# Optimization experiments

Measured on AMD Instinct MI355X. Metric: run time of the kernel, lower is better.

Reference implementation:

```python
import jax, jax.numpy as jnp
import numpy as np
import math

N_LEVELS = 8
PLANE_RES = 512
FEAT_DIM = 16
N_VERT = 10
N_SAMPLES = 262144
LEVEL_OFFSET = 0.0


def _projection_matrices():
    # planotic_solid vertices for n_vertices == 10 (half-dodecahedron)
    phi = (1.0 + math.sqrt(5.0)) / 2.0
    verts = np.array([
        [1.0, 1.0, 1.0], [1.0, 1.0, -1.0], [1.0, -1.0, 1.0], [1.0, -1.0, -1.0],
        [0.0, phi, 1.0 / phi], [0.0, phi, -1.0 / phi],
        [1.0 / phi, 0.0, phi], [1.0 / phi, 0.0, -phi],
        [phi, 1.0 / phi, 0.0], [phi, -1.0 / phi, 0.0]], dtype=np.float64)
    verts /= np.linalg.norm(verts, axis=-1, keepdims=True)
    Ps = []
    for a in verts:
        if a[0] != 0 or a[1] != 0:
            p0 = np.array([-a[1], a[0], 0.0])
        else:
            p0 = np.array([0.0, -a[2], a[1]])
        p1 = np.cross(a, p0)
        p0 /= np.linalg.norm(p0)
        p1 /= np.linalg.norm(p1)
        Ps.append(np.stack([p0, p1], axis=0))
    return np.stack(Ps, axis=0).astype(np.float32)  # (V, 2, 3)

P_MATS = _projection_matrices()

# static ripmap geometry: plane (l1, l2) has shape (H = res>>l2, W = res>>l1)
_W = np.array([PLANE_RES >> l for l in range(N_LEVELS)], dtype=np.int32)
_H = _W.copy()
_SIZES = np.array([int(_H[l2]) * int(_W[l1])
                   for l1 in range(N_LEVELS) for l2 in range(N_LEVELS)], dtype=np.int64)
_OFFS = np.concatenate([[0], np.cumsum(_SIZES)[:-1]]).astype(np.int32)


def build_ripmaps_flat(fm):
    """Build the 8x8 anisotropic mip pyramid and pack all planes into one flat buffer.
    fm: (V, H, W, F). Returns (V, total_pixels, F)."""
    flats = []
    base = fm
    for l1 in range(N_LEVELS):
        if l1 > 0:
            base = 0.5 * (base[:, :, 0::2] + base[:, :, 1::2])  # AvgPool (1,2): pool width
        cur = base
        for l2 in range(N_LEVELS):
            if l2 > 0:
                cur = 0.5 * (cur[:, 0::2] + cur[:, 1::2])        # AvgPool (2,1): pool height
            flats.append(cur.reshape(N_VERT, -1, FEAT_DIM))
    return jnp.concatenate(flats, axis=1)


def multi_anisomip_interp(flat, coords, level):
    """flat: (V, T, F) packed ripmaps; coords: (N, V, 2) in [-1, 1];
    level: (N, V, 2) fractional levels in [0, L-1].
    Quadrilinear: bilinear in space x bilinear across the (l1, l2) level grid."""
    W_arr = jnp.asarray(_W)
    H_arr = jnp.asarray(_H)
    off_arr = jnp.asarray(_OFFS)
    vidx = jnp.arange(N_VERT)[None, :]
    lx, ly = level[..., 0], level[..., 1]
    l1f_f = jnp.clip(jnp.floor(lx), 0.0, N_LEVELS - 1)
    l2f_f = jnp.clip(jnp.floor(ly), 0.0, N_LEVELS - 1)
    wx = jnp.clip(lx - l1f_f, 0.0, 1.0)
    wy = jnp.clip(ly - l2f_f, 0.0, 1.0)
    l1f = l1f_f.astype(jnp.int32)
    l2f = l2f_f.astype(jnp.int32)
    l1c = jnp.minimum(l1f + 1, N_LEVELS - 1)
    l2c = jnp.minimum(l2f + 1, N_LEVELS - 1)
    enc = jnp.zeros(coords.shape[:-1] + (FEAT_DIM,), dtype=flat.dtype)
    for l1, wl1 in ((l1f, 1.0 - wx), (l1c, wx)):
        Wl = W_arr[l1]  # (N, V)
        for l2, wl2 in ((l2f, 1.0 - wy), (l2c, wy)):
            Hl = H_arr[l2]
            off = off_arr[l1 * N_LEVELS + l2]
            u = (coords[..., 0] * 0.5 + 0.5) * Wl - 0.5
            v = (coords[..., 1] * 0.5 + 0.5) * Hl - 0.5
            uf = jnp.floor(u)
            vf = jnp.floor(v)
            fu = u - uf
            fv = v - vf
            ix0 = jnp.clip(uf.astype(jnp.int32), 0, Wl - 1)
            ix1 = jnp.clip(uf.astype(jnp.int32) + 1, 0, Wl - 1)
            iy0 = jnp.clip(vf.astype(jnp.int32), 0, Hl - 1)
            iy1 = jnp.clip(vf.astype(jnp.int32) + 1, 0, Hl - 1)
            wl = wl1 * wl2
            for ix, iy, wc in ((ix0, iy0, (1 - fu) * (1 - fv)),
                               (ix1, iy0, fu * (1 - fv)),
                               (ix0, iy1, (1 - fu) * fv),
                               (ix1, iy1, fu * fv)):
                idx = off + iy * Wl + ix  # (N, V) flat pixel index
                enc = enc + (wl * wc)[..., None] * flat[vidx, idx]
    return enc  # (N, V, F)


def setup_inputs() -> dict:
    key = jax.random.key(0)
    k1, k2, k3 = jax.random.split(key, 3)
    means = jax.random.uniform(k1, (N_SAMPLES, 3), minval=-1.0, maxval=1.0, dtype=jnp.float32)
    A = jax.random.normal(k2, (N_SAMPLES, 3, 3), dtype=jnp.float32) * 0.02
    covs = jnp.einsum('nij,nkj->nik', A, A) + 1e-10 * jnp.eye(3, dtype=jnp.float32)
    fm = jax.random.uniform(k3, (N_VERT, PLANE_RES, PLANE_RES, FEAT_DIM),
                            minval=-0.01, maxval=0.01, dtype=jnp.float32)
    return {"means": means, "covs": covs, "fm": fm}


def reference(means, covs, fm):
    P = jnp.asarray(P_MATS)                                   # (V, 2, 3)
    means_proj = jnp.einsum('nd,vcd->nvc', means, P)          # (N, V, 2)
    sig2 = jnp.einsum('vad,nde,vae->nva', P, covs, P)         # diag of P C P^T, (N, V, 2)
    sigmas = jnp.sqrt(jnp.maximum(sig2, 1e-20))
    level = jnp.log2(sigmas) + LEVEL_OFFSET + math.log2(PLANE_RES)
    level = jnp.clip(level, 0.0, N_LEVELS - 1)
    flat = build_ripmaps_flat(fm)
    enc = multi_anisomip_interp(flat, means_proj, level)      # (N, V, F)
    return enc.reshape(means.shape[0], N_VERT * FEAT_DIM)
```

## Files before the change

kernel.cpp:

```cpp
#include <hip/hip_runtime.h>
#include <hip/hip_fp16.h>


#define NV 10
#define FD 16
#define NS 262144
#define HALF_NS 131072
#define PYR_PX 1040400L
#define PYR_BYTES 332928000L
#define DUP0_PX 10404000
#define DUP_VPX 57600
#define OFF_PL 351360000L

__constant__ float c_P[NV][2][3] = {
  {{-0.7071067811865476f, 0.7071067811865476f, 0.0f},
   {-0.4082482904638631f,-0.4082482904638631f, 0.8164965809277261f}},
  {{-0.7071067811865476f, 0.7071067811865476f, 0.0f},
   { 0.4082482904638631f, 0.4082482904638631f, 0.8164965809277261f}},
  {{ 0.7071067811865476f, 0.7071067811865476f, 0.0f},
   {-0.4082482904638631f, 0.4082482904638631f, 0.8164965809277261f}},
  {{ 0.7071067811865476f, 0.7071067811865476f, 0.0f},
   { 0.4082482904638631f,-0.4082482904638631f, 0.8164965809277261f}},
  {{-1.0f, 0.0f, 0.0f},
   { 0.0f,-0.3568220897730899f, 0.9341723589627157f}},
  {{-1.0f, 0.0f, 0.0f},
   { 0.0f, 0.3568220897730899f, 0.9341723589627157f}},
  {{ 0.0f, 1.0f, 0.0f},
   {-0.9341723589627157f, 0.0f, 0.3568220897730899f}},
  {{ 0.0f, 1.0f, 0.0f},
   { 0.9341723589627157f, 0.0f, 0.3568220897730899f}},
  {{-0.3568220897730899f, 0.9341723589627157f, 0.0f},
   { 0.0f, 0.0f, 1.0f}},
  {{ 0.3568220897730899f, 0.9341723589627157f, 0.0f},
   { 0.0f, 0.0f, 1.0f}},
};

__constant__ int c_CW[8] = {0, 512, 768, 896, 960, 992, 1008, 1016};

__device__ __forceinline__ int offp_a(int l1, int l2) {
  return 1044480 - (1020 << (10 - l1)) + ((1024 - (1024 >> l2)) << (9 - l1));
}

__device__ __forceinline__ uint4 havg(uint4 a, uint4 c, __half2 hhalf) {
  uint4 res;
  __half2* rr = (__half2*)&res;
  const __half2* ha = (const __half2*)&a;
  const __half2* hc = (const __half2*)&c;
  #pragma unroll
  for (int j = 0; j < 4; ++j) rr[j] = __hmul2(__hadd2(ha[j], hc[j]), hhalf);
  return res;
}

__global__ __launch_bounds__(256) void build_all(const float* __restrict__ fm,
                                                 __half* __restrict__ pyr)
{
  __shared__ uint4 ldsA[2048];
  __shared__ uint4 ldsB[1024];
  int bid = blockIdx.x;
  int v = bid >> 8;
  int rem = bid & 255;
  int b = rem >> 2;
  int s = rem & 3;
  int t = threadIdx.x;

  __half* bv = pyr + (long)v * PYR_PX * FD;
  uint4* bv4 = (uint4*)bv;
  const __half2 hhalf = __floats2half2_rn(0.5f, 0.5f);

  {
    const float4* src = (const float4*)(fm +
        (((long)v * 512 + b * 8) * 512 + s * 128) * FD);
    uint2* ldsu2 = (uint2*)ldsA;
    #pragma unroll
    for (int i = 0; i < 16; ++i) {
      int u = t + 256 * i;
      int r = u >> 9;
      int f4 = u & 511;
      int px = f4 >> 2, qq = f4 & 3;
      float4 d = src[(long)r * 2048 + f4];
      __half2 h0 = __floats2half2_rn(d.x, d.y);
      __half2 h1 = __floats2half2_rn(d.z, d.w);
      uint2 val;
      val.x = *(unsigned*)&h0; val.y = *(unsigned*)&h1;
      ldsu2[(r * 128 + px) * 4 + qq] = val;
    }
  }
  __syncthreads();

  #pragma unroll
  for (int l1 = 0; l1 < 8; ++l1) {
    uint4* cur = (l1 & 1) ? ldsB : ldsA;
    const int Wc = 128 >> l1;

    if (l1 < 7) {
      uint4* nxt = (l1 & 1) ? ldsA : ldsB;
      const int Wn = Wc >> 1;
      const int units = 8 * Wn * 2;
      const int Wgn = 512 >> (l1 + 1);
      const int colbase = offp_a(l1 + 1, 0) + s * Wn;
      for (int u = t; u < units; u += 256) {
        int k = u & 1;
        int xr = u >> 1;
        int x = xr & (Wn - 1);
        int r = xr >> (6 - l1);
        uint4 a = cur[(r * Wc + 2 * x) * 2 + k];
        uint4 c = cur[(r * Wc + 2 * x + 1) * 2 + k];
        uint4 res = havg(a, c, hhalf);
        nxt[(r * Wn + x) * 2 + k] = res;
        bv4[(long)(colbase + (b * 8 + r) * Wgn + x) * 2 + k] = res;
      }
    }

    {
      const int slots = Wc * 2;
      if (t < slots) {
        int k = t & 1, x = t >> 1;
        const int Wg = 512 >> l1;
        uint4 r0 = cur[(0 * Wc + x) * 2 + k];
        uint4 r1 = cur[(1 * Wc + x) * 2 + k];
        uint4 r2 = cur[(2 * Wc + x) * 2 + k];
        uint4 r3 = cur[(3 * Wc + x) * 2 + k];
        uint4 r4 = cur[(4 * Wc + x) * 2 + k];
        uint4 r5 = cur[(5 * Wc + x) * 2 + k];
        uint4 r6 = cur[(6 * Wc + x) * 2 + k];
        uint4 r7 = cur[(7 * Wc + x) * 2 + k];
        uint4 a0 = havg(r0, r1, hhalf), a1 = havg(r2, r3, hhalf);
        uint4 a2 = havg(r4, r5, hhalf), a3 = havg(r6, r7, hhalf);
        uint4 b0 = havg(a0, a1, hhalf), b1 = havg(a2, a3, hhalf);
        uint4 c0 = havg(b0, b1, hhalf);
        int gx = s * Wc + x;
        long p1 = (long)offp_a(l1, 1) + (long)(b * 4) * Wg + gx;
        bv4[p1 * 2 + k] = a0;
        bv4[(p1 + Wg) * 2 + k] = a1;
        bv4[(p1 + 2 * Wg) * 2 + k] = a2;
        bv4[(p1 + 3 * Wg) * 2 + k] = a3;
        long p2 = (long)offp_a(l1, 2) + (long)(b * 2) * Wg + gx;
        bv4[p2 * 2 + k] = b0;
        bv4[(p2 + Wg) * 2 + k] = b1;
        long p3 = (long)offp_a(l1, 3) + (long)b * Wg + gx;
        bv4[p3 * 2 + k] = c0;
      }
    }
    __syncthreads();
  }
}

template<int L2SRC, int NLEV>
__global__ __launch_bounds__(256) void pool_hN(__half* __restrict__ pyr)
{
  constexpr int R = 1 << NLEV;
  constexpr int HL = 512 >> (L2SRC + NLEV);
  int total = NV * HL * 2040;
  int t = blockIdx.x * 256 + threadIdx.x;
  if (t >= total) return;
  int u = t % 2040;
  int r2 = t / 2040;
  int c = u >> 1, k = u & 1;
  int y = r2 % HL;
  int v = r2 / HL;
  int l1 = 0;
  #pragma unroll
  for (int i = 1; i < 8; ++i) l1 += (c >= c_CW[i]) ? 1 : 0;
  int x = c - c_CW[l1];
  int W = 512 >> l1;
  __half* bv = pyr + (long)v * PYR_PX * FD;
  const __half* src = bv + (long)offp_a(l1, L2SRC) * FD;

  uint4 d[R];
  long base = ((long)(y * R) * W + x) * FD + k * 8;
  #pragma unroll
  for (int r = 0; r < R; ++r)
    d[r] = *(const uint4*)(src + base + (long)r * W * FD);

  const __half2 hhalf = __floats2half2_rn(0.5f, 0.5f);
  #pragma unroll
  for (int lev = 1; lev <= NLEV; ++lev) {
    int cnt = R >> lev;
    __half* dst = bv + (long)offp_a(l1, L2SRC + lev) * FD;
    #pragma unroll
    for (int r = 0; r < cnt; ++r) {
      d[r] = havg(d[2 * r], d[2 * r + 1], hhalf);
      *(uint4*)(dst + (((long)(y * cnt + r)) * W + x) * FD + k * 8) = d[r];
    }
  }
}

__global__ __launch_bounds__(256) void build_dup(__half* __restrict__ pyr)
{
  int cb = blockIdx.y;
  int l1 = 2 + (cb >> 2), l2 = 2 + (cb & 3);
  int W = 512 >> l1, H = 512 >> l2;
  int units = NV * W * H * 2;
  int gx = blockIdx.x * 256 + threadIdx.x;
  if (gx >= units) return;
  int k = gx & 1;
  int p = gx >> 1;
  int x = p & (W - 1);
  int r = p >> (9 - l1);
  int y = r & (H - 1);
  int v = r >> (9 - l2);
  long srcPx = (long)v * PYR_PX + offp_a(l1, l2) + y * W + min(x + 1, W - 1);
  int Ad = 61440 - (245760 >> l1);
  int Bd = 256 - (1024 >> l2);
  long dstPx = (long)DUP0_PX + (long)v * DUP_VPX + Ad + ((Bd + y) << (9 - l1)) + x;
  const uint4* src = (const uint4*)(pyr + srcPx * FD);
  uint4* dst = (uint4*)(pyr + dstPx * FD);
  dst[k] = src[k];
}

__global__ __launch_bounds__(256) void proj_kernel(const float* __restrict__ means,
                                                   const float* __restrict__ covs,
                                                   float4* __restrict__ pl)
{
  int n = blockIdx.x * 256 + threadIdx.x;
  if (n >= NS) return;
  float m0 = means[3 * n], m1 = means[3 * n + 1], m2 = means[3 * n + 2];
  const float* C = covs + 9L * n;
  float c0 = C[0], c1 = C[1], c2 = C[2];
  float c3 = C[3], c4 = C[4], c5 = C[5];
  float c6 = C[6], c7 = C[7], c8 = C[8];
  #pragma unroll
  for (int v = 0; v < NV; ++v) {
    float p00 = c_P[v][0][0], p01 = c_P[v][0][1], p02 = c_P[v][0][2];
    float p10 = c_P[v][1][0], p11 = c_P[v][1][1], p12 = c_P[v][1][2];
    float cx = m0 * p00 + m1 * p01 + m2 * p02;
    float cy = m0 * p10 + m1 * p11 + m2 * p12;
    float t0 = c0 * p00 + c1 * p01 + c2 * p02;
    float t1 = c3 * p00 + c4 * p01 + c5 * p02;
    float t2 = c6 * p00 + c7 * p01 + c8 * p02;
    float s2x = p00 * t0 + p01 * t1 + p02 * t2;
    t0 = c0 * p10 + c1 * p11 + c2 * p12;
    t1 = c3 * p10 + c4 * p11 + c5 * p12;
    t2 = c6 * p10 + c7 * p11 + c8 * p12;
    float s2y = p10 * t0 + p11 * t1 + p12 * t2;
    float lx = 0.5f * log2f(fmaxf(s2x, 1e-20f)) + 9.0f;
    float ly = 0.5f * log2f(fmaxf(s2y, 1e-20f)) + 9.0f;
    lx = fminf(fmaxf(lx, 0.0f), 7.0f);
    ly = fminf(fmaxf(ly, 0.0f), 7.0f);
    pl[(long)v * NS + n] = make_float4(cx, cy, lx, ly);
  }
}

struct Ctx {
  int oA, oB, oC, oD, oE, oF, oG, oH;
  __half2 wA, wB, wC, wD, wE, wF, wG, wH;
  int z00;
  float fwA, fwB;
  int ix0, iy0, dy0;
};

__device__ __forceinline__ Ctx mk_ctx(const float4 p, const bool qodd,
                                      const int dupRel)
{
  Ctx c;
  float cx = p.x, cy = p.y, lx = p.z, ly = p.w;
  int l1f = (int)lx, l2f = (int)ly;
  float wx = lx - (float)l1f, wy = ly - (float)l2f;
  int l1c = min(l1f + 1, 7);
  int l2c = min(l2f + 1, 7);

  int sh_0 = 9 - l1f;
  int Ar_0 = 1044480 - (1020 << (10 - l1f));
  float u0 = (cx * 0.5f + 0.5f) * (float)(1 << sh_0) - 0.5f;
  float uf0 = floorf(u0);
  float fu0 = u0 - uf0;
  int iu0 = (int)uf0;
  bool e0 = (iu0 < 0) || (iu0 >= (1 << sh_0) - 1);
  int ix_0 = min(max(iu0, 0), (1 << sh_0) - 1);
  float wxl_0 = qodd ? (e0 ? 0.0f : fu0) : (e0 ? 1.0f : 1.0f - fu0);
  int pOdd_0 = ix_0 & 1;
  int Ad_0 = 61440 - (245760 >> l1f);
  int inR1_0 = ((unsigned)(l1f - 2) <= 3u) ? 1 : 0;

  int sh_1 = 9 - l1c;
  int Ar_1 = 1044480 - (1020 << (10 - l1c));
  float u1 = (cx * 0.5f + 0.5f) * (float)(1 << sh_1) - 0.5f;
  float uf1 = floorf(u1);
  float fu1 = u1 - uf1;
  int iu1 = (int)uf1;
  bool e1 = (iu1 < 0) || (iu1 >= (1 << sh_1) - 1);
  int ix_1 = min(max(iu1, 0), (1 << sh_1) - 1);
  float wxl_1 = qodd ? (e1 ? 0.0f : fu1) : (e1 ? 1.0f : 1.0f - fu1);
  int pOdd_1 = ix_1 & 1;
  int Ad_1 = 61440 - (245760 >> l1c);
  int inR1_1 = ((unsigned)(l1c - 2) <= 3u) ? 1 : 0;

  float wl1_0 = 1.0f - wx, wl1_1 = wx;

  int H0 = 512 >> l2f;
  float vv0 = (cy * 0.5f + 0.5f) * (float)H0 - 0.5f;
  float vf0 = floorf(vv0);
  float fv_0 = vv0 - vf0;
  int iv0 = (int)vf0;
  int iy_0 = min(max(iv0, 0), H0 - 1);
  int dy_0 = min(max(iv0 + 1, 0), H0 - 1) - iy_0;
  int Bv_0 = 1024 - (1024 >> l2f);
  int Bd_0 = 256 - (1024 >> l2f);
  int inR2_0 = ((unsigned)(l2f - 2) <= 3u) ? 1 : 0;

  int H1 = 512 >> l2c;
  float vv1 = (cy * 0.5f + 0.5f) * (float)H1 - 0.5f;
  float vf1 = floorf(vv1);
  float fv_1 = vv1 - vf1;
  int iv1 = (int)vf1;
  int iy_1 = min(max(iv1, 0), H1 - 1);
  int dy_1 = min(max(iv1 + 1, 0), H1 - 1) - iy_1;
  int Bv_1 = 1024 - (1024 >> l2c);
  int Bd_1 = 256 - (1024 >> l2c);
  int inR2_1 = ((unsigned)(l2c - 2) <= 3u) ? 1 : 0;

  float wl2_0 = 1.0f - wy, wl2_1 = wy;

  bool s00 = pOdd_0 && inR1_0 && inR2_0;
  c.oA = s00 ? (dupRel + Ad_0 + ((Bd_0 + iy_0) << sh_0) + ix_0 - 1)
             : (Ar_0 + ((Bv_0 + iy_0) << sh_0) + ix_0);
  c.oB = c.oA + (dy_0 << sh_0);
  bool s01 = pOdd_0 && inR1_0 && inR2_1;
  c.oC = s01 ? (dupRel + Ad_0 + ((Bd_1 + iy_1) << sh_0) + ix_0 - 1)
             : (Ar_0 + ((Bv_1 + iy_1) << sh_0) + ix_0);
  c.oD = c.oC + (dy_1 << sh_0);
  bool s10 = pOdd_1 && inR1_1 && inR2_0;
  c.oE = s10 ? (dupRel + Ad_1 + ((Bd_0 + iy_0) << sh_1) + ix_1 - 1)
             : (Ar_1 + ((Bv_0 + iy_0) << sh_1) + ix_1);
  c.oF = c.oE + (dy_0 << sh_1);
  bool s11 = pOdd_1 && inR1_1 && inR2_1;
  c.oG = s11 ? (dupRel + Ad_1 + ((Bd_1 + iy_1) << sh_1) + ix_1 - 1)
             : (Ar_1 + ((Bv_1 + iy_1) << sh_1) + ix_1);
  c.oH = c.oG + (dy_1 << sh_1);

  float wb00 = wl1_0 * wl2_0 * wxl_0;
  float wb01 = wl1_0 * wl2_1 * wxl_0;
  float wb10 = wl1_1 * wl2_0 * wxl_1;
  float wb11 = wl1_1 * wl2_1 * wxl_1;
  c.wA = __float2half2_rn(wb00 * (1.0f - fv_0));
  c.wB = __float2half2_rn(wb00 * fv_0);
  c.wC = __float2half2_rn(wb01 * (1.0f - fv_1));
  c.wD = __float2half2_rn(wb01 * fv_1);
  c.wE = __float2half2_rn(wb10 * (1.0f - fv_0));
  c.wF = __float2half2_rn(wb10 * fv_0);
  c.wG = __float2half2_rn(wb11 * (1.0f - fv_1));
  c.wH = __float2half2_rn(wb11 * fv_1);

  c.z00 = ((l1f | l2f) == 0) ? 1 : 0;
  c.fwA = wb00 * (1.0f - fv_0);
  c.fwB = wb00 * fv_0;
  c.ix0 = ix_0; c.iy0 = iy_0; c.dy0 = dy_0;
  if (c.z00) {
    __half2 z = __float2half2_rn(0.0f);
    c.wA = z; c.wB = z;
  }
  return c;
}

__global__ __launch_bounds__(256) void interp8(const float4* __restrict__ pl,
                                               const __half* __restrict__ pyr,
                                               const float* __restrict__ fm,
                                               float* __restrict__ out)
{
  int bid = blockIdx.x;
  int swz = (bid & 7) * 2560 + (bid >> 3);
  int t = swz * 256 + threadIdx.x;
  int q = t & 3;
  bool qodd = (q & 1);
  int vlow = (t >> 2) & 1;
  int n = (t >> 3) & (HALF_NS - 1);
  int v2 = t >> 20;
  int v = v2 * 2 + vlow;
  int nA = n, nB = n + HALF_NS;
  int dupRel = DUP0_PX + v * DUP_VPX - v * 1040400;

  float4 pA = pl[(long)v * NS + nA];
  float4 pB = pl[(long)v * NS + nB];

  const __half* bvq = pyr + (long)v * PYR_PX * FD + ((q & 1) * 16 + (q >> 1) * 8);

  Ctx cA = mk_ctx(pA, qodd, dupRel);
  uint4 dAA = *(const uint4*)(bvq + (long)cA.oA * FD);
  uint4 dAB = *(const uint4*)(bvq + (long)cA.oB * FD);
  uint4 dAC = *(const uint4*)(bvq + (long)cA.oC * FD);
  uint4 dAD = *(const uint4*)(bvq + (long)cA.oD * FD);
  uint4 dAE = *(const uint4*)(bvq + (long)cA.oE * FD);
  uint4 dAF = *(const uint4*)(bvq + (long)cA.oF * FD);
  uint4 dAG = *(const uint4*)(bvq + (long)cA.oG * FD);
  uint4 dAH = *(const uint4*)(bvq + (long)cA.oH * FD);

  Ctx cB = mk_ctx(pB, qodd, dupRel);
  uint4 dBA = *(const uint4*)(bvq + (long)cB.oA * FD);
  uint4 dBB = *(const uint4*)(bvq + (long)cB.oB * FD);
  uint4 dBC = *(const uint4*)(bvq + (long)cB.oC * FD);
  uint4 dBD = *(const uint4*)(bvq + (long)cB.oD * FD);
  uint4 dBE = *(const uint4*)(bvq + (long)cB.oE * FD);
  uint4 dBF = *(const uint4*)(bvq + (long)cB.oF * FD);
  uint4 dBG = *(const uint4*)(bvq + (long)cB.oG * FD);
  uint4 dBH = *(const uint4*)(bvq + (long)cB.oH * FD);
  __builtin_amdgcn_sched_barrier(0);

  __half2 z = __float2half2_rn(0.0f);
  __half2 aA0 = z, aA1 = z, aA2 = z, aA3 = z;
  __half2 aB0 = z, aB1 = z, aB2 = z, aB3 = z;
  #define ACC8(A0, A1, A2, A3, D, W) { const __half2* hh = (const __half2*)&(D); \
    A0 = __hfma2(hh[0], (W), A0); A1 = __hfma2(hh[1], (W), A1);                   \
    A2 = __hfma2(hh[2], (W), A2); A3 = __hfma2(hh[3], (W), A3); }
  ACC8(aA0,aA1,aA2,aA3, dAA, cA.wA) ACC8(aA0,aA1,aA2,aA3, dAB, cA.wB)
  ACC8(aA0,aA1,aA2,aA3, dAC, cA.wC) ACC8(aA0,aA1,aA2,aA3, dAD, cA.wD)
  ACC8(aA0,aA1,aA2,aA3, dAE, cA.wE) ACC8(aA0,aA1,aA2,aA3, dAF, cA.wF)
  ACC8(aA0,aA1,aA2,aA3, dAG, cA.wG) ACC8(aA0,aA1,aA2,aA3, dAH, cA.wH)
  ACC8(aB0,aB1,aB2,aB3, dBA, cB.wA) ACC8(aB0,aB1,aB2,aB3, dBB, cB.wB)
  ACC8(aB0,aB1,aB2,aB3, dBC, cB.wC) ACC8(aB0,aB1,aB2,aB3, dBD, cB.wD)
  ACC8(aB0,aB1,aB2,aB3, dBE, cB.wE) ACC8(aB0,aB1,aB2,aB3, dBF, cB.wF)
  ACC8(aB0,aB1,aB2,aB3, dBG, cB.wG) ACC8(aB0,aB1,aB2,aB3, dBH, cB.wH)
  #undef ACC8

  const float* fmv = fm + (long)v * (262144L * FD) + (q >> 1) * 8;
  if (cA.z00) {
    int px = min(cA.ix0 + (qodd ? 1 : 0), 511);
    long o0 = ((long)cA.iy0 * 512 + px) * FD;
    long o1 = o0 + (long)cA.dy0 * 512 * FD;
    float4 ga = *(const float4*)(fmv + o0);
    float4 gb = *(const float4*)(fmv + o0 + 4);
    float4 ha = *(const float4*)(fmv + o1);
    float4 hb = *(const float4*)(fmv + o1 + 4);
    __half2 hw0 = __float2half2_rn(cA.fwA);
    __half2 hw1 = __float2half2_rn(cA.fwB);
    aA0 = __hfma2(__floats2half2_rn(ga.x, ga.y), hw0, aA0);
    aA1 = __hfma2(__floats2half2_rn(ga.z, ga.w), hw0, aA1);
    aA2 = __hfma2(__floats2half2_rn(gb.x, gb.y), hw0, aA2);
    aA3 = __hfma2(__floats2half2_rn(gb.z, gb.w), hw0, aA3);
    aA0 = __hfma2(__floats2half2_rn(ha.x, ha.y), hw1, aA0);
    aA1 = __hfma2(__floats2half2_rn(ha.z, ha.w), hw1, aA1);
    aA2 = __hfma2(__floats2half2_rn(hb.x, hb.y), hw1, aA2);
    aA3 = __hfma2(__floats2half2_rn(hb.z, hb.w), hw1, aA3);
  }
  if (cB.z00) {
    int px = min(cB.ix0 + (qodd ? 1 : 0), 511);
    long o0 = ((long)cB.iy0 * 512 + px) * FD;
    long o1 = o0 + (long)cB.dy0 * 512 * FD;
    float4 ga = *(const float4*)(fmv + o0);
    float4 gb = *(const float4*)(fmv + o0 + 4);
    float4 ha = *(const float4*)(fmv + o1);
    float4 hb = *(const float4*)(fmv + o1 + 4);
    __half2 hw0 = __float2half2_rn(cB.fwA);
    __half2 hw1 = __float2half2_rn(cB.fwB);
    aB0 = __hfma2(__floats2half2_rn(ga.x, ga.y), hw0, aB0);
    aB1 = __hfma2(__floats2half2_rn(ga.z, ga.w), hw0, aB1);
    aB2 = __hfma2(__floats2half2_rn(gb.x, gb.y), hw0, aB2);
    aB3 = __hfma2(__floats2half2_rn(gb.z, gb.w), hw0, aB3);
    aB0 = __hfma2(__floats2half2_rn(ha.x, ha.y), hw1, aB0);
    aB1 = __hfma2(__floats2half2_rn(ha.z, ha.w), hw1, aB1);
    aB2 = __hfma2(__floats2half2_rn(hb.x, hb.y), hw1, aB2);
    aB3 = __hfma2(__floats2half2_rn(hb.z, hb.w), hw1, aB3);
  }

  #define XC(A0, A1, A2, A3) {                                   \
    int x0 = *(int*)&A0, x1 = *(int*)&A1;                        \
    int x2 = *(int*)&A2, x3 = *(int*)&A3;                        \
    int y0 = __shfl_xor(x0, 1), y1 = __shfl_xor(x1, 1);          \
    int y2 = __shfl_xor(x2, 1), y3 = __shfl_xor(x3, 1);          \
    A0 = __hadd2(A0, *(__half2*)&y0); A1 = __hadd2(A1, *(__half2*)&y1); \
    A2 = __hadd2(A2, *(__half2*)&y2); A3 = __hadd2(A3, *(__half2*)&y3); }
  XC(aA0, aA1, aA2, aA3)
  XC(aB0, aB1, aB2, aB3)
  #undef XC

  __half2 sA0 = qodd ? aA2 : aA0;
  __half2 sA1 = qodd ? aA3 : aA1;
  float2 fA0 = __half22float2(sA0);
  float2 fA1 = __half22float2(sA1);
  *(float4*)(out + ((long)nA * NV + v) * FD + q * 4) =
      make_float4(fA0.x, fA0.y, fA1.x, fA1.y);

  __half2 sB0 = qodd ? aB2 : aB0;
  __half2 sB1 = qodd ? aB3 : aB1;
  float2 fB0 = __half22float2(sB0);
  float2 fB1 = __half22float2(sB1);
  *(float4*)(out + ((long)nB * NV + v) * FD + q * 4) =
      make_float4(fB0.x, fB0.y, fB1.x, fB1.y);
}

extern "C" void kernel_launch(void* const* d_in, const int* in_sizes, int n_in,
                              void* d_out, int out_size, void* d_ws, size_t ws_size,
                              hipStream_t stream)
{
  const float* means = (const float*)d_in[0];
  const float* covs  = (const float*)d_in[1];
  const float* fm    = (const float*)d_in[2];
  float* out = (float*)d_out;
  __half* pyr = (__half*)d_ws;
  float4* pl  = (float4*)((char*)d_ws + OFF_PL);

  build_all<<<NV * 256, 256, 0, stream>>>(fm, pyr);
  {
    int tB = NV * 8 * 2040;
    pool_hN<3, 3><<<(tB + 255) / 256, 256, 0, stream>>>(pyr);
    int tC = NV * 4 * 2040;
    pool_hN<6, 1><<<(tC + 255) / 256, 256, 0, stream>>>(pyr);
  }
  {
    dim3 g(1280, 16, 1);
    build_dup<<<g, 256, 0, stream>>>(pyr);
  }
  proj_kernel<<<(NS + 255) / 256, 256, 0, stream>>>(means, covs, pl);

  interp8<<<20480, 256, 0, stream>>>(pl, pyr, fm, out);
}
```

Baseline: 251.2 us.

## Skip building level-0 ripmap rows; handle low-level samples in a fixup pass

Stops writing the l1=0 and l2=0 pyramid planes (full-resolution column and row mips), which cuts pyramid construction traffic. Samples whose level is below 1 on either axis are collected into a list with a global atomic in the projection kernel. A new fixup kernel then recomputes those samples by averaging directly from the fp32 feature map, and the main interpolation kernel zeroes the weights that would have read the missing planes. The cost is atomic contention, an extra kernel, and per-sample strided gathers that loop over up to 128 source texels for coarse levels.

```diff
diff --git a/kernel.cpp b/kernel.cpp
--- a/kernel.cpp
+++ b/kernel.cpp
@@ -7,10 +7,11 @@
 #define NS 262144
 #define HALF_NS 131072
 #define PYR_PX 1040400L
-#define PYR_BYTES 332928000L
 #define DUP0_PX 10404000
 #define DUP_VPX 57600
-#define OFF_PL 351360000L
+#define OFF_PL   351360000L
+#define OFF_CNT  393303040L
+#define OFF_LIST 393303104L
 
 __constant__ float c_P[NV][2][3] = {
   {{-0.7071067811865476f, 0.7071067811865476f, 0.0f},
@@ -96,8 +97,6 @@
       uint4* nxt = (l1 & 1) ? ldsA : ldsB;
       const int Wn = Wc >> 1;
       const int units = 8 * Wn * 2;
-      const int Wgn = 512 >> (l1 + 1);
-      const int colbase = offp_a(l1 + 1, 0) + s * Wn;
       for (int u = t; u < units; u += 256) {
         int k = u & 1;
         int xr = u >> 1;
@@ -105,13 +104,11 @@
         int r = xr >> (6 - l1);
         uint4 a = cur[(r * Wc + 2 * x) * 2 + k];
         uint4 c = cur[(r * Wc + 2 * x + 1) * 2 + k];
-        uint4 res = havg(a, c, hhalf);
-        nxt[(r * Wn + x) * 2 + k] = res;
-        bv4[(long)(colbase + (b * 8 + r) * Wgn + x) * 2 + k] = res;
+        nxt[(r * Wn + x) * 2 + k] = havg(a, c, hhalf);
       }
     }
 
-    {
+    if (l1 >= 1) {
       const int slots = Wc * 2;
       if (t < slots) {
         int k = t & 1, x = t >> 1;
@@ -150,12 +147,12 @@
 {
   constexpr int R = 1 << NLEV;
   constexpr int HL = 512 >> (L2SRC + NLEV);
-  int total = NV * HL * 2040;
+  int total = NV * HL * 1016;
   int t = blockIdx.x * 256 + threadIdx.x;
   if (t >= total) return;
-  int u = t % 2040;
-  int r2 = t / 2040;
-  int c = u >> 1, k = u & 1;
+  int u = t % 1016;
+  int r2 = t / 1016;
+  int c = 512 + (u >> 1), k = u & 1;
   int y = r2 % HL;
   int v = r2 / HL;
   int l1 = 0;
@@ -210,7 +207,9 @@
 
 __global__ __launch_bounds__(256) void proj_kernel(const float* __restrict__ means,
                                                    const float* __restrict__ covs,
-                                                   float4* __restrict__ pl)
+                                                   float4* __restrict__ pl,
+                                                   int* __restrict__ cnt,
+                                                   int* __restrict__ list)
 {
   int n = blockIdx.x * 256 + threadIdx.x;
   if (n >= NS) return;
@@ -238,15 +237,16 @@
     lx = fminf(fmaxf(lx, 0.0f), 7.0f);
     ly = fminf(fmaxf(ly, 0.0f), 7.0f);
     pl[(long)v * NS + n] = make_float4(cx, cy, lx, ly);
+    if (lx < 1.0f || ly < 1.0f) {
+      int pos = atomicAdd(cnt, 1);
+      list[pos] = v * NS + n;
+    }
   }
 }
 
 struct Ctx {
   int oA, oB, oC, oD, oE, oF, oG, oH;
   __half2 wA, wB, wC, wD, wE, wF, wG, wH;
-  int z00;
-  float fwA, fwB;
-  int ix0, iy0, dy0;
 };
 
 __device__ __forceinline__ Ctx mk_ctx(const float4 p, const bool qodd,
@@ -341,20 +341,14 @@
   c.wG = __float2half2_rn(wb11 * (1.0f - fv_1));
   c.wH = __float2half2_rn(wb11 * fv_1);
 
-  c.z00 = ((l1f | l2f) == 0) ? 1 : 0;
-  c.fwA = wb00 * (1.0f - fv_0);
-  c.fwB = wb00 * fv_0;
-  c.ix0 = ix_0; c.iy0 = iy_0; c.dy0 = dy_0;
-  if (c.z00) {
-    __half2 z = __float2half2_rn(0.0f);
-    c.wA = z; c.wB = z;
-  }
+  __half2 z = __float2half2_rn(0.0f);
+  if (l1f == 0) { c.wA = z; c.wB = z; c.wC = z; c.wD = z; }
+  if (l2f == 0) { c.wA = z; c.wB = z; c.wE = z; c.wF = z; }
   return c;
 }
 
 __global__ __launch_bounds__(256) void interp8(const float4* __restrict__ pl,
                                                const __half* __restrict__ pyr,
-                                               const float* __restrict__ fm,
                                                float* __restrict__ out)
 {
   int bid = blockIdx.x;
@@ -411,46 +405,6 @@
   ACC8(aB0,aB1,aB2,aB3, dBG, cB.wG) ACC8(aB0,aB1,aB2,aB3, dBH, cB.wH)
   #undef ACC8
 
-  const float* fmv = fm + (long)v * (262144L * FD) + (q >> 1) * 8;
-  if (cA.z00) {
-    int px = min(cA.ix0 + (qodd ? 1 : 0), 511);
-    long o0 = ((long)cA.iy0 * 512 + px) * FD;
-    long o1 = o0 + (long)cA.dy0 * 512 * FD;
-    float4 ga = *(const float4*)(fmv + o0);
-    float4 gb = *(const float4*)(fmv + o0 + 4);
-    float4 ha = *(const float4*)(fmv + o1);
-    float4 hb = *(const float4*)(fmv + o1 + 4);
-    __half2 hw0 = __float2half2_rn(cA.fwA);
-    __half2 hw1 = __float2half2_rn(cA.fwB);
-    aA0 = __hfma2(__floats2half2_rn(ga.x, ga.y), hw0, aA0);
-    aA1 = __hfma2(__floats2half2_rn(ga.z, ga.w), hw0, aA1);
-    aA2 = __hfma2(__floats2half2_rn(gb.x, gb.y), hw0, aA2);
-    aA3 = __hfma2(__floats2half2_rn(gb.z, gb.w), hw0, aA3);
-    aA0 = __hfma2(__floats2half2_rn(ha.x, ha.y), hw1, aA0);
-    aA1 = __hfma2(__floats2half2_rn(ha.z, ha.w), hw1, aA1);
-    aA2 = __hfma2(__floats2half2_rn(hb.x, hb.y), hw1, aA2);
-    aA3 = __hfma2(__floats2half2_rn(hb.z, hb.w), hw1, aA3);
-  }
-  if (cB.z00) {
-    int px = min(cB.ix0 + (qodd ? 1 : 0), 511);
-    long o0 = ((long)cB.iy0 * 512 + px) * FD;
-    long o1 = o0 + (long)cB.dy0 * 512 * FD;
-    float4 ga = *(const float4*)(fmv + o0);
-    float4 gb = *(const float4*)(fmv + o0 + 4);
-    float4 ha = *(const float4*)(fmv + o1);
-    float4 hb = *(const float4*)(fmv + o1 + 4);
-    __half2 hw0 = __float2half2_rn(cB.fwA);
-    __half2 hw1 = __float2half2_rn(cB.fwB);
-    aB0 = __hfma2(__floats2half2_rn(ga.x, ga.y), hw0, aB0);
-    aB1 = __hfma2(__floats2half2_rn(ga.z, ga.w), hw0, aB1);
-    aB2 = __hfma2(__floats2half2_rn(gb.x, gb.y), hw0, aB2);
-    aB3 = __hfma2(__floats2half2_rn(gb.z, gb.w), hw0, aB3);
-    aB0 = __hfma2(__floats2half2_rn(ha.x, ha.y), hw1, aB0);
-    aB1 = __hfma2(__floats2half2_rn(ha.z, ha.w), hw1, aB1);
-    aB2 = __hfma2(__floats2half2_rn(hb.x, hb.y), hw1, aB2);
-    aB3 = __hfma2(__floats2half2_rn(hb.z, hb.w), hw1, aB3);
-  }
-
   #define XC(A0, A1, A2, A3) {                                   \
     int x0 = *(int*)&A0, x1 = *(int*)&A1;                        \
     int x2 = *(int*)&A2, x3 = *(int*)&A3;                        \
@@ -477,6 +431,111 @@
       make_float4(fB0.x, fB0.y, fB1.x, fB1.y);
 }
 
+__global__ __launch_bounds__(256) void fixup(const float4* __restrict__ pl,
+                                             const __half* __restrict__ pyr,
+                                             const float* __restrict__ fm,
+                                             const int* __restrict__ cnt,
+                                             const int* __restrict__ list,
+                                             float* __restrict__ out)
+{
+  int nfix = *cnt;
+  int q = threadIdx.x & 3;
+  bool qodd = (q & 1);
+  int stride = (gridDim.x * 256) >> 2;
+  for (int idx = (blockIdx.x * 256 + threadIdx.x) >> 2; idx < nfix; idx += stride) {
+    int pv = list[idx];
+    int v = pv >> 18;
+    int n = pv & (NS - 1);
+    float4 p = pl[(long)pv];
+    float cx = p.x, cy = p.y, lx = p.z, ly = p.w;
+    int l1f = (int)lx, l2f = (int)ly;
+    float wx = lx - (float)l1f, wy = ly - (float)l2f;
+    int l1c = min(l1f + 1, 7), l2c = min(l2f + 1, 7);
+    const float* fmv = fm + (long)v * (262144L * FD) + (q >> 1) * 8;
+    const __half* bv = pyr + (long)v * PYR_PX * FD + (q >> 1) * 8;
+    float a0=0,a1=0,a2=0,a3=0,a4=0,a5=0,a6=0,a7=0;
+
+    #pragma unroll
+    for (int ii = 0; ii < 2; ++ii) {
+      int l1 = ii ? l1c : l1f;
+      float wl1 = ii ? wx : 1.0f - wx;
+      int Wl = 512 >> l1;
+      float u = (cx * 0.5f + 0.5f) * (float)Wl - 0.5f;
+      float uf = floorf(u);
+      float fu = u - uf;
+      int iu = (int)uf;
+      int ix0 = min(max(iu, 0), Wl - 1);
+      int ix1 = min(max(iu + 1, 0), Wl - 1);
+      bool xe = (ix1 == ix0);
+      float wxl = qodd ? (xe ? 0.0f : fu) : (xe ? 1.0f : 1.0f - fu);
+      int myx = qodd ? ix1 : ix0;
+      #pragma unroll
+      for (int jj = 0; jj < 2; ++jj) {
+        int l2 = jj ? l2c : l2f;
+        float wl2 = jj ? wy : 1.0f - wy;
+        int Hl = 512 >> l2;
+        float vv = (cy * 0.5f + 0.5f) * (float)Hl - 0.5f;
+        float vf = floorf(vv);
+        float fv = vv - vf;
+        int iv = (int)vf;
+        int iy0 = min(max(iv, 0), Hl - 1);
+        int iy1 = min(max(iv + 1, 0), Hl - 1);
+        float wb = wl1 * wl2 * wxl;
+        float tw0 = wb * (1.0f - fv), tw1 = wb * fv;
+        #pragma unroll
+        for (int tt = 0; tt < 2; ++tt) {
+          int iy = tt ? iy1 : iy0;
+          float w = tt ? tw1 : tw0;
+          if (w == 0.0f) continue;
+          float s0=0,s1=0,s2=0,s3=0,s4=0,s5=0,s6=0,s7=0;
+          if (l1 > 0 && l2 > 0) {
+            const __half* pp = bv + ((long)offp_a(l1, l2) + (long)iy * Wl + myx) * FD;
+            uint4 d = *(const uint4*)pp;
+            const __half2* hh = (const __half2*)&d;
+            float2 f0 = __half22float2(hh[0]), f1 = __half22float2(hh[1]);
+            float2 f2 = __half22float2(hh[2]), f3 = __half22float2(hh[3]);
+            s0=f0.x; s1=f0.y; s2=f1.x; s3=f1.y; s4=f2.x; s5=f2.y; s6=f3.x; s7=f3.y;
+          } else if (l1 == 0 && l2 == 0) {
+            const float* s = fmv + ((long)iy * 512 + myx) * FD;
+            float4 g0 = *(const float4*)s, g1 = *(const float4*)(s + 4);
+            s0=g0.x; s1=g0.y; s2=g0.z; s3=g0.w; s4=g1.x; s5=g1.y; s6=g1.z; s7=g1.w;
+          } else if (l2 == 0) {
+            int base = myx << l1, m = 1 << l1;
+            for (int c2 = 0; c2 < m; ++c2) {
+              const float* s = fmv + ((long)iy * 512 + base + c2) * FD;
+              float4 g0 = *(const float4*)s, g1 = *(const float4*)(s + 4);
+              s0+=g0.x; s1+=g0.y; s2+=g0.z; s3+=g0.w;
+              s4+=g1.x; s5+=g1.y; s6+=g1.z; s7+=g1.w;
+            }
+            float inv = 1.0f / (float)m;
+            s0*=inv; s1*=inv; s2*=inv; s3*=inv; s4*=inv; s5*=inv; s6*=inv; s7*=inv;
+          } else {
+            int base = iy << l2, m = 1 << l2;
+            for (int r2 = 0; r2 < m; ++r2) {
+              const float* s = fmv + ((long)(base + r2) * 512 + myx) * FD;
+              float4 g0 = *(const float4*)s, g1 = *(const float4*)(s + 4);
+              s0+=g0.x; s1+=g0.y; s2+=g0.z; s3+=g0.w;
+              s4+=g1.x; s5+=g1.y; s6+=g1.z; s7+=g1.w;
+            }
+            float inv = 1.0f / (float)m;
+            s0*=inv; s1*=inv; s2*=inv; s3*=inv; s4*=inv; s5*=inv; s6*=inv; s7*=inv;
+          }
+          a0+=w*s0; a1+=w*s1; a2+=w*s2; a3+=w*s3;
+          a4+=w*s4; a5+=w*s5; a6+=w*s6; a7+=w*s7;
+        }
+      }
+    }
+
+    a0 += __shfl_xor(a0, 1); a1 += __shfl_xor(a1, 1);
+    a2 += __shfl_xor(a2, 1); a3 += __shfl_xor(a3, 1);
+    a4 += __shfl_xor(a4, 1); a5 += __shfl_xor(a5, 1);
+    a6 += __shfl_xor(a6, 1); a7 += __shfl_xor(a7, 1);
+
+    float4 o = qodd ? make_float4(a4, a5, a6, a7) : make_float4(a0, a1, a2, a3);
+    *(float4*)(out + ((long)n * NV + v) * FD + q * 4) = o;
+  }
+}
+
 extern "C" void kernel_launch(void* const* d_in, const int* in_sizes, int n_in,
                               void* d_out, int out_size, void* d_ws, size_t ws_size,
                               hipStream_t stream)
@@ -487,19 +546,23 @@
   float* out = (float*)d_out;
   __half* pyr = (__half*)d_ws;
   float4* pl  = (float4*)((char*)d_ws + OFF_PL);
-
+  int* cnt    = (int*)((char*)d_ws + OFF_CNT);
+  int* list   = (int*)((char*)d_ws + OFF_LIST);
+
+  hipMemsetAsync(cnt, 0, 4, stream);
   build_all<<<NV * 256, 256, 0, stream>>>(fm, pyr);
   {
-    int tB = NV * 8 * 2040;
+    int tB = NV * 8 * 1016;
     pool_hN<3, 3><<<(tB + 255) / 256, 256, 0, stream>>>(pyr);
-    int tC = NV * 4 * 2040;
+    int tC = NV * 4 * 1016;
     pool_hN<6, 1><<<(tC + 255) / 256, 256, 0, stream>>>(pyr);
   }
   {
     dim3 g(1280, 16, 1);
     build_dup<<<g, 256, 0, stream>>>(pyr);
   }
-  proj_kernel<<<(NS + 255) / 256, 256, 0, stream>>>(means, covs, pl);
-
-  interp8<<<20480, 256, 0, stream>>>(pl, pyr, fm, out);
-}
+  proj_kernel<<<(NS + 255) / 256, 256, 0, stream>>>(means, covs, pl, cnt, list);
+
+  interp8<<<20480, 256, 0, stream>>>(pl, pyr, out);
+  fixup<<<256, 256, 0, stream>>>(pl, pyr, fm, cnt, list, out);
+}
```

Measured after the change: 444.9 us. 1.77x slower.
